# Performance work log

Measured on AMD Instinct MI355X. Metric: run time of the kernel, lower is better.

Reference implementation:

```python
import jax, jax.numpy as jnp
import numpy as np

# DWMTJ / LI constants (from RecNet defaults; dwmtjrec source not shipped, see notes)
DT = 1e-10          # integration timestep [s]
ALPHA = 100.0       # SuperSpike surrogate sharpness ('super' method)
HLEAK = 0.0         # leak field -> position leak coefficient
W2 = 2.5e-8         # track length / firing threshold on DW position [m]
I_APP = 1e-4        # applied bias current [A]
MU = 2.5e5          # DW mobility: velocity per unit current [m/(A*s)]
TAU_MEM_INV = 100.0 # LI readout membrane 1/tau [1/s] (norse defaults)
TAU_SYN_INV = 200.0 # LI readout synaptic 1/tau [1/s]


@jax.custom_vjp
def superspike(x):
    # Heaviside spike with SuperSpike surrogate gradient (method='super')
    return (x > 0).astype(x.dtype)

def _ss_fwd(x):
    return superspike(x), x

def _ss_bwd(x, g):
    return (g / (ALPHA * jnp.abs(x) + 1.0) ** 2,)

superspike.defvjp(_ss_fwd, _ss_bwd)


def setup_inputs() -> dict:
    key = jax.random.key(0)
    k1, k2, k3, k4 = jax.random.split(key, 4)
    T, B, C, H, W = 100, 256, 2, 34, 34
    IN, HID, OUT = C * H * W, 512, 10  # IN = 2312
    x = jax.random.uniform(k1, (T, B, C, H, W), dtype=jnp.float32)
    w_in = jax.random.normal(k2, (HID, IN), jnp.float32) / np.sqrt(IN).astype(np.float32)
    w_rec = jax.random.normal(k3, (HID, HID), jnp.float32) / np.sqrt(HID).astype(np.float32)
    w_out = jax.random.normal(k4, (OUT, HID), jnp.float32) / np.sqrt(HID).astype(np.float32)
    return {"x": x, "w_in": w_in, "w_rec": w_rec, "w_out": w_out}


def reference(x, w_in, w_rec, w_out):
    T = x.shape[0]
    IN, HID = w_in.shape[1], w_in.shape[0]
    OUT = w_out.shape[0]
    xs = x.reshape(T, -1, IN)  # [T, Bflat, IN] -- matches .view(-1, input_features)
    Bf = xs.shape[1]

    def step(state, zt):
        pos, z, v, i_syn = state
        # DWMTJ recurrent cell: input + recurrent drive + applied bias current
        cur = zt @ w_in.T + z @ w_rec.T + I_APP                 # [Bf, HID]
        pos = pos + DT * (MU * cur - HLEAK * pos)               # DW position update
        z_new = superspike(pos - W2)                            # fire at track end
        pos = pos * (1.0 - z_new)                               # reset position
        # readout linear (no bias) then leaky-integrate (norse LICell)
        inp = z_new @ w_out.T                                   # [Bf, OUT]
        v_new = v + DT * TAU_MEM_INV * (-v + i_syn)
        i_new = i_syn + DT * TAU_SYN_INV * (-i_syn) + inp
        return (pos, z_new, v_new, i_new), v_new

    zeros_h = jnp.zeros((Bf, HID), x.dtype)
    zeros_o = jnp.zeros((Bf, OUT), x.dtype)
    s0 = (zeros_h, zeros_h, zeros_o, zeros_o)
    _, voltages = jax.lax.scan(step, s0, xs)  # [T, Bf, OUT]
    return voltages
```

## Files before the change

kernel.cpp:

```cpp
#include <hip/hip_runtime.h>
#include <cstdint>
#include <cstddef>

#define TSTEPS 100
#define NB 256
#define INF 2312
#define HIDN 512
#define NOUT 10
#define BKT 73

#define OFF_WT  0
#define OFF_ZB  262144
#define OFF_CTR 327680
#define OFF_CI  328704
#define WS_FLOATS 13435904

typedef double f64x4 __attribute__((ext_vector_type(4)));
typedef float  f32x4 __attribute__((ext_vector_type(4)));
typedef short  short8 __attribute__((ext_vector_type(8)));

__device__ __forceinline__ void dpos_f64(int di, int lane, int r, int& m, int& n) {
    const int l16 = lane & 15, kq = lane >> 4;
    switch (di) {
    case 0:  m = 4 * kq + r;         n = l16;                break;
    case 1:  m = l16;                n = 4 * kq + r;         break;
    case 2:  m = kq + 4 * r;         n = l16;                break;
    case 3:  m = l16;                n = kq + 4 * r;         break;
    case 4:  m = lane >> 2;          n = 4 * (lane & 3) + r; break;
    default: n = lane >> 2;          m = 4 * (lane & 3) + r; break;
    }
}

__device__ __forceinline__ void bsplit(float x, unsigned short& h1,
                                       unsigned short& h2, unsigned short& h3) {
    unsigned int xb = __float_as_uint(x);
    h1 = (unsigned short)(xb >> 16);
    float r1 = x - __uint_as_float(xb & 0xFFFF0000u);
    unsigned int r1b = __float_as_uint(r1);
    h2 = (unsigned short)(r1b >> 16);
    float r2 = r1 - __uint_as_float(r1b & 0xFFFF0000u);
    h3 = (unsigned short)(__float_as_uint(r2) >> 16);
}

__global__ __launch_bounds__(256) void init_kernel(float* __restrict__ ws,
                                                   const float* __restrict__ w_rec) {
    int n = blockIdx.x * 256 + threadIdx.x;
    if (n < HIDN * HIDN) {
        int j = n >> 9, h = n & 511;
        ws[n] = w_rec[h * HIDN + j];
    } else if (n < OFF_CI) {
        ws[n] = 0.0f;
    }
}

__global__ __launch_bounds__(64) void probe_kernel(unsigned int* __restrict__ mode_out) {
    const int l = threadIdx.x;
    __shared__ unsigned int maskls;
    if (l == 0) maskls = 0xFFFFFFu;
    __syncthreads();
    double a1v = 1.0 + 3.0 * (double)l, b1v = 2.0 + 5.0 * (double)l;
    double a2v = 7.0 - 2.0 * (double)l, b2v = -3.0 + (double)l;
    f64x4 pacc;
#pragma unroll
    for (int r = 0; r < 4; ++r) pacc[r] = 1000.0 * r + 17.0 * l;
    pacc = __builtin_amdgcn_mfma_f64_16x16x4f64(a1v, b1v, pacc, 0, 0, 0);
    pacc = __builtin_amdgcn_mfma_f64_16x16x4f64(a2v, b2v, pacc, 0, 0, 0);
    unsigned int my = 0;
    for (int ai = 0; ai < 2; ++ai)
        for (int bi = 0; bi < 2; ++bi)
            for (int di = 0; di < 6; ++di) {
                bool ok = true;
                for (int r = 0; r < 4; ++r) {
                    int m, n; dpos_f64(di, l, r, m, n);
                    double e = 1000.0 * r + 17.0 * l;
                    for (int k = 0; k < 4; ++k) {
                        int lA = ai ? (4 * m + k) : (m + 16 * k);
                        int lB = bi ? (4 * n + k) : (n + 16 * k);
                        e += (1.0 + 3.0 * (double)lA) * (2.0 + 5.0 * (double)lB)
                           + (7.0 - 2.0 * (double)lA) * (-3.0 + (double)lB);
                    }
                    ok = ok && (pacc[r] == e);
                }
                if (ok) my |= 1u << (ai * 12 + bi * 6 + di);
            }
    atomicAnd(&maskls, my);
    __syncthreads();
    if (l == 0) mode_out[0] = maskls ? (unsigned)(__ffs((int)maskls) - 1) : 255u;
}

__global__ __launch_bounds__(64) void probe_bf(unsigned int* __restrict__ out) {
    const int l = threadIdx.x;
    __shared__ unsigned int maskls;
    if (l == 0) maskls = 0xFFu;
    __syncthreads();
    short8 a1v, a2v, b1v, b2v;
#pragma unroll
    for (int j = 0; j < 8; ++j) {
        a1v[j] = (short)(__float_as_uint((float)(1 + l + 2 * j)) >> 16);
        b1v[j] = (short)(__float_as_uint((float)(2 + 2 * l + 3 * j)) >> 16);
        a2v[j] = (short)(__float_as_uint((float)(5 - l + j)) >> 16);
        b2v[j] = (short)(__float_as_uint((float)(-3 + l - 2 * j)) >> 16);
    }
    f32x4 pacc;
#pragma unroll
    for (int r = 0; r < 4; ++r) pacc[r] = (float)(1000 * r + 17 * l);
    pacc = __builtin_amdgcn_mfma_f32_16x16x32_bf16(a1v, b1v, pacc, 0, 0, 0);
    pacc = __builtin_amdgcn_mfma_f32_16x16x32_bf16(a2v, b2v, pacc, 0, 0, 0);
    unsigned int my = 0;
    for (int combo = 0; combo < 8; ++combo) {
        const int ai = combo >> 2, bi = (combo >> 1) & 1, dd = combo & 1;
        bool ok = true;
        for (int r = 0; r < 4; ++r) {
            int mm = dd ? (l & 15) : (4 * (l >> 4) + r);
            int nn = dd ? (4 * (l >> 4) + r) : (l & 15);
            double e = 1000.0 * r + 17.0 * l;
            for (int k = 0; k < 32; ++k) {
                int lA = ai ? (4 * mm + (k >> 3)) : (mm + 16 * (k >> 3));
                int lB = bi ? (4 * nn + (k >> 3)) : (nn + 16 * (k >> 3));
                int jj = k & 7;
                e += (double)((1 + lA + 2 * jj) * (2 + 2 * lB + 3 * jj)
                            + (5 - lA + jj) * (-3 + lB - 2 * jj));
            }
            ok = ok && ((double)pacc[r] == e);
        }
        if (ok) my |= 1u << combo;
    }
    atomicAnd(&maskls, my);
    __syncthreads();
    if (l == 0) out[0] = maskls ? (unsigned)(__ffs((int)maskls) - 1) : 255u;
}

__global__ __launch_bounds__(256, 3) void gemm_bf(const float* __restrict__ X,
        const float* __restrict__ Win, float* __restrict__ C,
        const unsigned int* __restrict__ bfp) {
    const unsigned int bm = bfp[0];
    if (bm >= 8u) return;
    __shared__ unsigned int Au[3][64 * 20];
    __shared__ unsigned int Bu[3][128 * 20];
    const int tid = threadIdx.x;
    const int lane = tid & 63, wv = tid >> 6;
    const int a_m  = (bm & 4) ? (lane >> 2) : (lane & 15);
    const int a_kb = (bm & 4) ? (lane & 3)  : (lane >> 4);
    const int b_n  = (bm & 2) ? (lane >> 2) : (lane & 15);
    const int b_kb = (bm & 2) ? (lane & 3)  : (lane >> 4);
    const int di = (int)(bm & 1);
    const int row0 = blockIdx.y * 64, col0 = blockIdx.x * 128;
    const int sra = tid >> 2, ska = (tid & 3) * 8;
    const int srb = tid >> 1, skb = (tid & 1) * 16;

    double accd[8][4] = {};

    for (int kt = 0; kt < BKT; ++kt) {
        const int k0 = kt * 32;
        __syncthreads();
        {
            unsigned short h1[8], h2[8], h3[8];
#pragma unroll
            for (int q = 0; q < 2; ++q) {
                int gk = k0 + ska + q * 4;
                float4 v = make_float4(0.f, 0.f, 0.f, 0.f);
                if (gk < INF)
                    v = *(const float4*)(X + (size_t)(row0 + sra) * INF + gk);
                bsplit(v.x, h1[q*4+0], h2[q*4+0], h3[q*4+0]);
                bsplit(v.y, h1[q*4+1], h2[q*4+1], h3[q*4+1]);
                bsplit(v.z, h1[q*4+2], h2[q*4+2], h3[q*4+2]);
                bsplit(v.w, h1[q*4+3], h2[q*4+3], h3[q*4+3]);
            }
            const int ab = sra * 20 + (ska >> 1);
#pragma unroll
            for (int e = 0; e < 2; ++e) {
                uint2 p;
                p.x = (unsigned)h1[e*4+0] | ((unsigned)h1[e*4+1] << 16);
                p.y = (unsigned)h1[e*4+2] | ((unsigned)h1[e*4+3] << 16);
                *(uint2*)&Au[0][ab + e*2] = p;
                p.x = (unsigned)h2[e*4+0] | ((unsigned)h2[e*4+1] << 16);
                p.y = (unsigned)h2[e*4+2] | ((unsigned)h2[e*4+3] << 16);
                *(uint2*)&Au[1][ab + e*2] = p;
                p.x = (unsigned)h3[e*4+0] | ((unsigned)h3[e*4+1] << 16);
                p.y = (unsigned)h3[e*4+2] | ((unsigned)h3[e*4+3] << 16);
                *(uint2*)&Au[2][ab + e*2] = p;
            }
        }
        {
            unsigned short g1[16], g2[16], g3[16];
#pragma unroll
            for (int q = 0; q < 4; ++q) {
                int gk = k0 + skb + q * 4;
                float4 v = make_float4(0.f, 0.f, 0.f, 0.f);
                if (gk < INF)
                    v = *(const float4*)(Win + (size_t)(col0 + srb) * INF + gk);
                bsplit(v.x, g1[q*4+0], g2[q*4+0], g3[q*4+0]);
                bsplit(v.y, g1[q*4+1], g2[q*4+1], g3[q*4+1]);
                bsplit(v.z, g1[q*4+2], g2[q*4+2], g3[q*4+2]);
                bsplit(v.w, g1[q*4+3], g2[q*4+3], g3[q*4+3]);
            }
            const int bb = srb * 20 + (skb >> 1);
#pragma unroll
            for (int e = 0; e < 4; ++e) {
                uint2 p;
                p.x = (unsigned)g1[e*4+0] | ((unsigned)g1[e*4+1] << 16);
                p.y = (unsigned)g1[e*4+2] | ((unsigned)g1[e*4+3] << 16);
                *(uint2*)&Bu[0][bb + e*2] = p;
                p.x = (unsigned)g2[e*4+0] | ((unsigned)g2[e*4+1] << 16);
                p.y = (unsigned)g2[e*4+2] | ((unsigned)g2[e*4+3] << 16);
                *(uint2*)&Bu[1][bb + e*2] = p;
                p.x = (unsigned)g3[e*4+0] | ((unsigned)g3[e*4+1] << 16);
                p.y = (unsigned)g3[e*4+2] | ((unsigned)g3[e*4+3] << 16);
                *(uint2*)&Bu[2][bb + e*2] = p;
            }
        }
        __syncthreads();
        const int ar = (wv * 16 + a_m) * 20 + a_kb * 4;
        short8 fa1 = *(short8*)&Au[0][ar];
        short8 fa2 = *(short8*)&Au[1][ar];
        short8 fa3 = *(short8*)&Au[2][ar];
#pragma unroll
        for (int nt = 0; nt < 8; ++nt) {
            const int br = (nt * 16 + b_n) * 20 + b_kb * 4;
            short8 fb1 = *(short8*)&Bu[0][br];
            short8 fb2 = *(short8*)&Bu[1][br];
            short8 fb3 = *(short8*)&Bu[2][br];
            f32x4 acc = {0.f, 0.f, 0.f, 0.f};
            acc = __builtin_amdgcn_mfma_f32_16x16x32_bf16(fa3, fb2, acc, 0, 0, 0);
            acc = __builtin_amdgcn_mfma_f32_16x16x32_bf16(fa2, fb3, acc, 0, 0, 0);
            acc = __builtin_amdgcn_mfma_f32_16x16x32_bf16(fa3, fb1, acc, 0, 0, 0);
            acc = __builtin_amdgcn_mfma_f32_16x16x32_bf16(fa2, fb2, acc, 0, 0, 0);
            acc = __builtin_amdgcn_mfma_f32_16x16x32_bf16(fa1, fb3, acc, 0, 0, 0);
            acc = __builtin_amdgcn_mfma_f32_16x16x32_bf16(fa2, fb1, acc, 0, 0, 0);
            acc = __builtin_amdgcn_mfma_f32_16x16x32_bf16(fa1, fb2, acc, 0, 0, 0);
            acc = __builtin_amdgcn_mfma_f32_16x16x32_bf16(fa1, fb1, acc, 0, 0, 0);
            accd[nt][0] += (double)acc[0]; accd[nt][1] += (double)acc[1];
            accd[nt][2] += (double)acc[2]; accd[nt][3] += (double)acc[3];
        }
    }
#pragma unroll
    for (int nt = 0; nt < 8; ++nt)
#pragma unroll
        for (int r = 0; r < 4; ++r) {
            int m = di ? (lane & 15) : (4 * (lane >> 4) + r);
            int n = di ? (4 * (lane >> 4) + r) : (lane & 15);
            C[(size_t)(row0 + wv * 16 + m) * HIDN + col0 + nt * 16 + n]
                = (float)accd[nt][r];
        }
}

__global__ __launch_bounds__(256, 3) void gemm_mfma3(const float* __restrict__ X,
        const float* __restrict__ Win, float* __restrict__ C,
        const unsigned int* __restrict__ modep, const unsigned int* __restrict__ bfp) {
    if (bfp[0] < 8u) return;
    const unsigned int mode = modep[0];
    if (mode >= 24u) return;
    const int di = (int)(mode % 6u), bi = (int)((mode / 6u) & 1u), ai = (int)(mode / 12u);
    __shared__ float As[32][72];
    __shared__ float Bs[32][144];
    const int tid = threadIdx.x;
    const int lane = tid & 63, wv = tid >> 6;
    const int a_m = ai ? (lane >> 2) : (lane & 15);
    const int a_k = ai ? (lane & 3) : (lane >> 4);
    const int b_n = bi ? (lane >> 2) : (lane & 15);
    const int b_k = bi ? (lane & 3) : (lane >> 4);
    const int row0 = blockIdx.y * 64, col0 = blockIdx.x * 128;
    const int sra = tid >> 2, ska = (tid & 3) * 8;
    const int srb = tid >> 1, skb = (tid & 1) * 16;

    float4 va[2], vb[4];
#pragma unroll
    for (int q = 0; q < 2; ++q)
        va[q] = *(const float4*)(X + (size_t)(row0 + sra) * INF + ska + q * 4);
#pragma unroll
    for (int q = 0; q < 4; ++q)
        vb[q] = *(const float4*)(Win + (size_t)(col0 + srb) * INF + skb + q * 4);

    f64x4 acc[8] = {};
    for (int k0 = 0; k0 < INF; k0 += 32) {
        __syncthreads();
#pragma unroll
        for (int q = 0; q < 2; ++q) {
            int kc = ska + q * 4;
            As[kc + 0][sra] = va[q].x; As[kc + 1][sra] = va[q].y;
            As[kc + 2][sra] = va[q].z; As[kc + 3][sra] = va[q].w;
        }
#pragma unroll
        for (int q = 0; q < 4; ++q) {
            int kc = skb + q * 4;
            Bs[kc + 0][srb] = vb[q].x; Bs[kc + 1][srb] = vb[q].y;
            Bs[kc + 2][srb] = vb[q].z; Bs[kc + 3][srb] = vb[q].w;
        }
        __syncthreads();
        const int kn = k0 + 32;
        if (kn < INF) {
#pragma unroll
            for (int q = 0; q < 2; ++q) {
                int gk = kn + ska + q * 4;
                float4 a = make_float4(0.f, 0.f, 0.f, 0.f);
                if (gk < INF)
                    a = *(const float4*)(X + (size_t)(row0 + sra) * INF + gk);
                va[q] = a;
            }
#pragma unroll
            for (int q = 0; q < 4; ++q) {
                int gk = kn + skb + q * 4;
                float4 b = make_float4(0.f, 0.f, 0.f, 0.f);
                if (gk < INF)
                    b = *(const float4*)(Win + (size_t)(col0 + srb) * INF + gk);
                vb[q] = b;
            }
        }
#pragma unroll
        for (int s = 0; s < 8; ++s) {
            double a = (double)As[s * 4 + a_k][wv * 16 + a_m];
#pragma unroll
            for (int nt = 0; nt < 8; ++nt) {
                double b = (double)Bs[s * 4 + b_k][nt * 16 + b_n];
                acc[nt] = __builtin_amdgcn_mfma_f64_16x16x4f64(a, b, acc[nt], 0, 0, 0);
            }
        }
    }
#pragma unroll
    for (int nt = 0; nt < 8; ++nt)
#pragma unroll
        for (int r = 0; r < 4; ++r) {
            int m, n; dpos_f64(di, lane, r, m, n);
            C[(size_t)(row0 + wv * 16 + m) * HIDN + col0 + nt * 16 + n]
                = (float)acc[nt][r];
        }
}

__global__ __launch_bounds__(256, 2) void gemm_vec(const float* __restrict__ X,
        const float* __restrict__ Win, float* __restrict__ C,
        const unsigned int* __restrict__ modep, const unsigned int* __restrict__ bfp) {
    if (bfp[0] < 8u || modep[0] < 24u) return;
    __shared__ double As[32][130];
    __shared__ double Bs[32][144];
    const int tid = threadIdx.x;
    const int tx = tid & 15;
    const int ty = tid >> 4;
    const int row0 = blockIdx.y * 128, col0 = blockIdx.x * 128;
    const int sr = tid >> 1, sk = (tid & 1) * 16;
    const int srz = sr + (sr >> 3);
    float4 va[4], vb[4];
#pragma unroll
    for (int q = 0; q < 4; ++q) {
        int gk = sk + q * 4;
        va[q] = *(const float4*)(X + (size_t)(row0 + sr) * INF + gk);
        vb[q] = *(const float4*)(Win + (size_t)(col0 + sr) * INF + gk);
    }
    double acc[8][8] = {};
    for (int k0 = 0; k0 < INF; k0 += 32) {
        __syncthreads();
#pragma unroll
        for (int q = 0; q < 4; ++q) {
            int kc = sk + q * 4;
            As[kc + 0][sr] = (double)va[q].x; As[kc + 1][sr] = (double)va[q].y;
            As[kc + 2][sr] = (double)va[q].z; As[kc + 3][sr] = (double)va[q].w;
            Bs[kc + 0][srz] = (double)vb[q].x; Bs[kc + 1][srz] = (double)vb[q].y;
            Bs[kc + 2][srz] = (double)vb[q].z; Bs[kc + 3][srz] = (double)vb[q].w;
        }
        __syncthreads();
        const int kn = k0 + 32;
        if (kn < INF) {
#pragma unroll
            for (int q = 0; q < 4; ++q) {
                int gk = kn + sk + q * 4;
                float4 a = make_float4(0.f, 0.f, 0.f, 0.f);
                float4 b = make_float4(0.f, 0.f, 0.f, 0.f);
                if (gk < INF) {
                    a = *(const float4*)(X + (size_t)(row0 + sr) * INF + gk);
                    b = *(const float4*)(Win + (size_t)(col0 + sr) * INF + gk);
                }
                va[q] = a; vb[q] = b;
            }
        }
#pragma unroll 4
        for (int kk = 0; kk < 32; ++kk) {
            double ad[8], bd[8];
#pragma unroll
            for (int i = 0; i < 8; ++i) ad[i] = As[kk][ty * 8 + i];
#pragma unroll
            for (int j = 0; j < 8; ++j) bd[j] = Bs[kk][9 * tx + j];
#pragma unroll
            for (int i = 0; i < 8; ++i)
#pragma unroll
                for (int j = 0; j < 8; ++j)
                    acc[i][j] += ad[i] * bd[j];
        }
    }
#pragma unroll
    for (int i = 0; i < 8; ++i) {
#pragma unroll
        for (int jj = 0; jj < 2; ++jj) {
            float4 o;
            o.x = (float)acc[i][jj * 4 + 0]; o.y = (float)acc[i][jj * 4 + 1];
            o.z = (float)acc[i][jj * 4 + 2]; o.w = (float)acc[i][jj * 4 + 3];
            *(float4*)(C + (size_t)(row0 + ty * 8 + i) * HIDN + col0 + tx * 8 + jj * 4) = o;
        }
    }
}

__global__ __launch_bounds__(512) void fused_tag(const float* __restrict__ ci,
        const float* __restrict__ wT, const float* __restrict__ w_out,
        float* __restrict__ out, unsigned char* __restrict__ zb) {
    __shared__ float zfb[4096];
    __shared__ float wout2[2][512];
    const int tid = threadIdx.x;
    const int wv = tid >> 6, lane = tid & 63;
    const int i = (int)blockIdx.x;
    const int c = (i >> 3) & 7;
    const int g = (i & 7) | ((i >> 6) << 3);
    const int b0 = g * 8;

    float wreg[64];
#pragma unroll
    for (int qq = 0; qq < 64; ++qq)
        wreg[qq] = wT[(size_t)((wv << 6) + qq) * HIDN + (c << 6) + lane];

    if (tid < 512) {
        wout2[0][tid] = w_out[c * HIDN + tid];
        wout2[1][tid] = (c < 2) ? w_out[(8 + c) * HIDN + tid] : 0.0f;
    }
    for (int idx = tid; idx < 4096; idx += 512) zfb[idx] = 0.0f;
    __syncthreads();

    unsigned char* zbA = zb + (size_t)b0 * HIDN;
    unsigned char* zbB = zb + 131072 + (size_t)b0 * HIDN;

    float pos = 0.0f;
    float vA = 0.f, iA = 0.f, vB = 0.f, iB = 0.f;

    for (int t = 0; t < TSTEPS; ++t) {
        float f[8] = {0.f, 0.f, 0.f, 0.f, 0.f, 0.f, 0.f, 0.f};
#pragma unroll
        for (int q4 = 0; q4 < 16; ++q4) {
            float4 z4[8];
#pragma unroll
            for (int b = 0; b < 8; ++b)
                z4[b] = *(const float4*)&zfb[b * 512 + (wv << 6) + q4 * 4];
#pragma unroll
            for (int b = 0; b < 8; ++b) {
                f[b] = __fmaf_rn(z4[b].x, wreg[q4 * 4 + 0], f[b]);
                f[b] = __fmaf_rn(z4[b].y, wreg[q4 * 4 + 1], f[b]);
                f[b] = __fmaf_rn(z4[b].z, wreg[q4 * 4 + 2], f[b]);
                f[b] = __fmaf_rn(z4[b].w, wreg[q4 * 4 + 3], f[b]);
            }
        }
        __syncthreads();
#pragma unroll
        for (int b = 0; b < 8; ++b)
            zfb[((wv << 3) + b) * 64 + lane] = f[b];
        __syncthreads();

        double acc = 0.0;
#pragma unroll
        for (int c2 = 0; c2 < 8; ++c2)
            acc += (double)zfb[((c2 << 3) + wv) * 64 + lane];
        float rec32 = (float)acc;
        float civ = ci[((size_t)t * NB + (b0 + wv)) * HIDN + (c << 6) + lane];
        float cur = __fadd_rn(__fadd_rn(civ, rec32), 1e-4f);
        float mc = __fmul_rn(2.5e5f, cur);
        pos = __fadd_rn(pos, __fmul_rn(1e-10f, mc));
        bool zbit = __fsub_rn(pos, 2.5e-8f) > 0.0f;
        pos = zbit ? 0.0f : pos;
        unsigned char* zw = (t & 1) ? zbB : zbA;
        const unsigned int tag2 = ((unsigned)(t >> 1) + 1u) << 1;
        __hip_atomic_store(&zw[wv * HIDN + (c << 6) + lane],
                           (unsigned char)(tag2 | (zbit ? 1u : 0u)),
                           __ATOMIC_RELAXED, __HIP_MEMORY_SCOPE_AGENT);
        __syncthreads();

        {
            const int bb = tid >> 6, j8 = (tid & 63) * 8;
            const unsigned char* zr = zw + bb * HIDN + j8;
            const unsigned int t2b = tag2 * 0x01010101u;
            unsigned int vx, vy;
            for (;;) {
                vx = __hip_atomic_load((const unsigned int*)zr,
                                       __ATOMIC_RELAXED, __HIP_MEMORY_SCOPE_AGENT);
                vy = __hip_atomic_load((const unsigned int*)(zr + 4),
                                       __ATOMIC_RELAXED, __HIP_MEMORY_SCOPE_AGENT);
                if (((vx & 0xFEFEFEFEu) == t2b) && ((vy & 0xFEFEFEFEu) == t2b))
                    break;
                __builtin_amdgcn_s_sleep(1);
            }
            float4 o0, o1;
            o0.x = (float)(vx & 1u);         o0.y = (float)((vx >> 8) & 1u);
            o0.z = (float)((vx >> 16) & 1u); o0.w = (float)((vx >> 24) & 1u);
            o1.x = (float)(vy & 1u);         o1.y = (float)((vy >> 8) & 1u);
            o1.z = (float)((vy >> 16) & 1u); o1.w = (float)((vy >> 24) & 1u);
            *(float4*)&zfb[bb * 512 + j8] = o0;
            *(float4*)&zfb[bb * 512 + j8 + 4] = o1;
        }
        __syncthreads();

#pragma unroll
        for (int oo = 0; oo < 2; ++oo) {
            int o = (oo == 0) ? c : (c < 2 ? 8 + c : -1);
            if (o < 0) continue;
            double part = 0.0;
#pragma unroll
            for (int c2 = 0; c2 < 8; ++c2) {
                double zfv = (double)zfb[wv * 512 + (c2 << 6) + lane];
                part = __fma_rn(zfv, (double)wout2[oo][(c2 << 6) + lane], part);
            }
#pragma unroll
            for (int off = 32; off > 0; off >>= 1) part += __shfl_down(part, off);
            if (lane == 0) {
                float inp = (float)part;
                float vvv = (oo == 0) ? vA : vB;
                float iiv = (oo == 0) ? iA : iB;
                float vn = __fadd_rn(vvv, __fmul_rn(1e-8f, __fsub_rn(iiv, vvv)));
                float t2 = __fmul_rn(2e-8f, iiv);
                float in2 = __fadd_rn(__fsub_rn(iiv, t2), inp);
                if (oo == 0) { vA = vn; iA = in2; } else { vB = vn; iB = in2; }
                out[((size_t)t * NB + (b0 + wv)) * NOUT + o] = vn;
            }
        }
    }
}

extern "C" void kernel_launch(void* const* d_in, const int* in_sizes, int n_in,
                              void* d_out, int out_size, void* d_ws, size_t ws_size,
                              hipStream_t stream) {
    (void)in_sizes; (void)n_in; (void)out_size;
    const float* x     = (const float*)d_in[0];
    const float* w_in  = (const float*)d_in[1];
    const float* w_rec = (const float*)d_in[2];
    const float* w_out = (const float*)d_in[3];
    float* out = (float*)d_out;
    float* ws  = (float*)d_ws;
    if (ws_size < (size_t)WS_FLOATS * 4) return;

    float* wT = ws + OFF_WT;
    unsigned char* zb = (unsigned char*)(ws + OFF_ZB);
    unsigned int* ctr = (unsigned int*)(ws + OFF_CTR);
    unsigned int* bfmode = ctr + 1022;
    unsigned int* mode = ctr + 1023;
    float* ci = ws + OFF_CI;

    hipLaunchKernelGGL(init_kernel, dim3((OFF_CI + 255) / 256), dim3(256), 0,
                       stream, ws, w_rec);
    hipLaunchKernelGGL(probe_kernel, dim3(1), dim3(64), 0, stream, mode);
    hipLaunchKernelGGL(probe_bf, dim3(1), dim3(64), 0, stream, bfmode);
    hipLaunchKernelGGL(gemm_bf, dim3(4, 400), dim3(256), 0, stream,
                       x, w_in, ci, bfmode);
    hipLaunchKernelGGL(gemm_mfma3, dim3(4, 400), dim3(256), 0, stream,
                       x, w_in, ci, mode, bfmode);
    hipLaunchKernelGGL(gemm_vec, dim3(4, 200), dim3(256), 0, stream,
                       x, w_in, ci, mode, bfmode);
    hipLaunchKernelGGL(fused_tag, dim3(NB), dim3(512), 0, stream,
                       ci, wT, w_out, out, zb);
}
```

Baseline: 1.136 ms.

## Pre-split W_in into bf16 planes and read B fragments directly from global

Adds a pre-pass that splits W_in once into three padded bf16 planes (hi/mid/lo). A new GEMM kernel then loads the B fragments straight from those planes in global memory, with no per-tile split and no LDS staging of B. This removes the repeated bsplit work on W_in across the 400 row blocks, shrinks LDS use, and raises the occupancy hint to 4 blocks. In exchange it depends on a larger workspace: the old kernel is used as a fallback when the workspace is too small, and the uncoalesced B loads now rely on L2 hits.

```diff
diff --git a/kernel.cpp b/kernel.cpp
--- a/kernel.cpp
+++ b/kernel.cpp
@@ -8,12 +8,16 @@
 #define HIDN 512
 #define NOUT 10
 #define BKT 73
+#define KPAD 2336
+#define PL (512 * KPAD)
 
 #define OFF_WT  0
 #define OFF_ZB  262144
 #define OFF_CTR 327680
 #define OFF_CI  328704
 #define WS_FLOATS 13435904
+#define OFF_WB  13435904
+#define WS_FLOATS_FULL (13435904 + 1794048)
 
 typedef double f64x4 __attribute__((ext_vector_type(4)));
 typedef float  f32x4 __attribute__((ext_vector_type(4)));
@@ -50,6 +54,29 @@
         ws[n] = w_rec[h * HIDN + j];
     } else if (n < OFF_CI) {
         ws[n] = 0.0f;
+    }
+}
+
+__global__ __launch_bounds__(256) void split_win(const float* __restrict__ Win,
+                                                 unsigned short* __restrict__ wb) {
+    int idx = blockIdx.x * 256 + threadIdx.x;
+    if (idx >= 512 * (KPAD / 8)) return;
+    int col = idx / (KPAD / 8), k = (idx - col * (KPAD / 8)) * 8;
+    unsigned short h1[8], h2[8], h3[8];
+#pragma unroll
+    for (int j = 0; j < 8; ++j) {
+        float v = (k + j < INF) ? Win[(size_t)col * INF + k + j] : 0.0f;
+        bsplit(v, h1[j], h2[j], h3[j]);
+    }
+#pragma unroll
+    for (int p = 0; p < 3; ++p) {
+        const unsigned short* hp = (p == 0) ? h1 : (p == 1) ? h2 : h3;
+        uint4 o;
+        o.x = (unsigned)hp[0] | ((unsigned)hp[1] << 16);
+        o.y = (unsigned)hp[2] | ((unsigned)hp[3] << 16);
+        o.z = (unsigned)hp[4] | ((unsigned)hp[5] << 16);
+        o.w = (unsigned)hp[6] | ((unsigned)hp[7] << 16);
+        *(uint4*)&wb[(size_t)p * PL + (size_t)col * KPAD + k] = o;
     }
 }
 
@@ -130,6 +157,93 @@
     if (l == 0) out[0] = maskls ? (unsigned)(__ffs((int)maskls) - 1) : 255u;
 }
 
+__global__ __launch_bounds__(256, 4) void gemm_bf2(const float* __restrict__ X,
+        const unsigned short* __restrict__ wb, float* __restrict__ C,
+        const unsigned int* __restrict__ bfp) {
+    const unsigned int bm = bfp[0];
+    if (bm >= 8u) return;
+    __shared__ unsigned int Au[3][64 * 20];
+    const int tid = threadIdx.x;
+    const int lane = tid & 63, wv = tid >> 6;
+    const int a_m  = (bm & 4) ? (lane >> 2) : (lane & 15);
+    const int a_kb = (bm & 4) ? (lane & 3)  : (lane >> 4);
+    const int b_n  = (bm & 2) ? (lane >> 2) : (lane & 15);
+    const int b_kb = (bm & 2) ? (lane & 3)  : (lane >> 4);
+    const int di = (int)(bm & 1);
+    const int row0 = blockIdx.y * 64, col0 = blockIdx.x * 128;
+    const int sra = tid >> 2, ska = (tid & 3) * 8;
+
+    unsigned int cb[8];
+#pragma unroll
+    for (int nt = 0; nt < 8; ++nt)
+        cb[nt] = (unsigned)(col0 + nt * 16 + b_n) * KPAD + b_kb * 8;
+
+    double accd[8][4] = {};
+
+    for (int kt = 0; kt < BKT; ++kt) {
+        const int k0 = kt * 32;
+        __syncthreads();
+        {
+            unsigned short h1[8], h2[8], h3[8];
+#pragma unroll
+            for (int q = 0; q < 2; ++q) {
+                int gk = k0 + ska + q * 4;
+                float4 v = make_float4(0.f, 0.f, 0.f, 0.f);
+                if (gk < INF)
+                    v = *(const float4*)(X + (size_t)(row0 + sra) * INF + gk);
+                bsplit(v.x, h1[q*4+0], h2[q*4+0], h3[q*4+0]);
+                bsplit(v.y, h1[q*4+1], h2[q*4+1], h3[q*4+1]);
+                bsplit(v.z, h1[q*4+2], h2[q*4+2], h3[q*4+2]);
+                bsplit(v.w, h1[q*4+3], h2[q*4+3], h3[q*4+3]);
+            }
+            const int ab = sra * 20 + (ska >> 1);
+#pragma unroll
+            for (int e = 0; e < 2; ++e) {
+                uint2 p;
+                p.x = (unsigned)h1[e*4+0] | ((unsigned)h1[e*4+1] << 16);
+                p.y = (unsigned)h1[e*4+2] | ((unsigned)h1[e*4+3] << 16);
+                *(uint2*)&Au[0][ab + e*2] = p;
+                p.x = (unsigned)h2[e*4+0] | ((unsigned)h2[e*4+1] << 16);
+                p.y = (unsigned)h2[e*4+2] | ((unsigned)h2[e*4+3] << 16);
+                *(uint2*)&Au[1][ab + e*2] = p;
+                p.x = (unsigned)h3[e*4+0] | ((unsigned)h3[e*4+1] << 16);
+                p.y = (unsigned)h3[e*4+2] | ((unsigned)h3[e*4+3] << 16);
+                *(uint2*)&Au[2][ab + e*2] = p;
+            }
+        }
+        __syncthreads();
+        const int ar = (wv * 16 + a_m) * 20 + a_kb * 4;
+        short8 fa1 = *(short8*)&Au[0][ar];
+        short8 fa2 = *(short8*)&Au[1][ar];
+        short8 fa3 = *(short8*)&Au[2][ar];
+#pragma unroll
+        for (int nt = 0; nt < 8; ++nt) {
+            const size_t ba = (size_t)cb[nt] + (unsigned)k0;
+            short8 fb1 = *(const short8*)&wb[ba];
+            short8 fb2 = *(const short8*)&wb[(size_t)PL + ba];
+            short8 fb3 = *(const short8*)&wb[(size_t)(2 * PL) + ba];
+            f32x4 acc = {0.f, 0.f, 0.f, 0.f};
+            acc = __builtin_amdgcn_mfma_f32_16x16x32_bf16(fa3, fb1, acc, 0, 0, 0);
+            acc = __builtin_amdgcn_mfma_f32_16x16x32_bf16(fa2, fb2, acc, 0, 0, 0);
+            acc = __builtin_amdgcn_mfma_f32_16x16x32_bf16(fa1, fb3, acc, 0, 0, 0);
+            acc = __builtin_amdgcn_mfma_f32_16x16x32_bf16(fa2, fb1, acc, 0, 0, 0);
+            acc = __builtin_amdgcn_mfma_f32_16x16x32_bf16(fa1, fb2, acc, 0, 0, 0);
+            acc = __builtin_amdgcn_mfma_f32_16x16x32_bf16(fa1, fb1, acc, 0, 0, 0);
+            accd[nt][0] += (double)acc[0]; accd[nt][1] += (double)acc[1];
+            accd[nt][2] += (double)acc[2]; accd[nt][3] += (double)acc[3];
+        }
+    }
+#pragma unroll
+    for (int nt = 0; nt < 8; ++nt)
+#pragma unroll
+        for (int r = 0; r < 4; ++r) {
+            int m = di ? (lane & 15) : (4 * (lane >> 4) + r);
+            int n = di ? (4 * (lane >> 4) + r) : (lane & 15);
+            C[(size_t)(row0 + wv * 16 + m) * HIDN + col0 + nt * 16 + n]
+                = (float)accd[nt][r];
+        }
+}
+
 __global__ __launch_bounds__(256, 3) void gemm_bf(const float* __restrict__ X,
         const float* __restrict__ Win, float* __restrict__ C,
         const unsigned int* __restrict__ bfp) {
@@ -149,7 +263,6 @@
     const int srb = tid >> 1, skb = (tid & 1) * 16;
 
     double accd[8][4] = {};
-
     for (int kt = 0; kt < BKT; ++kt) {
         const int k0 = kt * 32;
         __syncthreads();
@@ -528,6 +641,7 @@
     float* out = (float*)d_out;
     float* ws  = (float*)d_ws;
     if (ws_size < (size_t)WS_FLOATS * 4) return;
+    const bool haveWB = ws_size >= (size_t)WS_FLOATS_FULL * 4;
 
     float* wT = ws + OFF_WT;
     unsigned char* zb = (unsigned char*)(ws + OFF_ZB);
@@ -535,13 +649,21 @@
     unsigned int* bfmode = ctr + 1022;
     unsigned int* mode = ctr + 1023;
     float* ci = ws + OFF_CI;
+    unsigned short* wb = (unsigned short*)(ws + OFF_WB);
 
     hipLaunchKernelGGL(init_kernel, dim3((OFF_CI + 255) / 256), dim3(256), 0,
                        stream, ws, w_rec);
     hipLaunchKernelGGL(probe_kernel, dim3(1), dim3(64), 0, stream, mode);
     hipLaunchKernelGGL(probe_bf, dim3(1), dim3(64), 0, stream, bfmode);
-    hipLaunchKernelGGL(gemm_bf, dim3(4, 400), dim3(256), 0, stream,
-                       x, w_in, ci, bfmode);
+    if (haveWB) {
+        hipLaunchKernelGGL(split_win, dim3((512 * (KPAD / 8) + 255) / 256),
+                           dim3(256), 0, stream, w_in, wb);
+        hipLaunchKernelGGL(gemm_bf2, dim3(4, 400), dim3(256), 0, stream,
+                           x, wb, ci, bfmode);
+    } else {
+        hipLaunchKernelGGL(gemm_bf, dim3(4, 400), dim3(256), 0, stream,
+                           x, w_in, ci, bfmode);
+    }
     hipLaunchKernelGGL(gemm_mfma3, dim3(4, 400), dim3(256), 0, stream,
                        x, w_in, ci, mode, bfmode);
     hipLaunchKernelGGL(gemm_vec, dim3(4, 200), dim3(256), 0, stream,
```

Measured after the change: 1.596 ms. +40.5%, slower.
